# Performance work log

Measured on AMD Instinct MI355X. Metric: run time of the kernel, lower is better.

## Reference

```python
import jax, jax.numpy as jnp
import numpy as np

B, N, DEG = 128, 512, 8          # graphs, nodes per graph, avg degree
E = B * N * DEG                  # 524288 edges
F_IN, H1, H2, C = 128, 64, 128, 10
RATIO = 0.8
K = int(np.ceil(RATIO * N))      # TopKPooling keeps ceil(0.8*N)=410 nodes per graph


def setup_inputs() -> dict:
    key = jax.random.key(0)
    ks = jax.random.split(key, 10)
    n_nodes = B * N
    x = jax.random.normal(ks[0], (n_nodes, F_IN), dtype=jnp.float32)
    # random intra-graph edges, then offset node ids per graph
    src = jax.random.randint(ks[1], (B, N * DEG), 0, N)
    dst = jax.random.randint(ks[2], (B, N * DEG), 0, N)
    off = (jnp.arange(B) * N)[:, None]
    edge_index = jnp.stack([(src + off).reshape(-1), (dst + off).reshape(-1)]).astype(jnp.int64)
    batch = jnp.repeat(jnp.arange(B), N).astype(jnp.int64)
    s1 = 1.0 / np.sqrt(F_IN)
    s2 = 1.0 / np.sqrt(H1)
    s3 = 1.0 / np.sqrt(H2)
    return {
        "x": x,
        "edge_index": edge_index,
        "batch": batch,
        "W1": jax.random.uniform(ks[3], (F_IN, H1), jnp.float32, -s1, s1),
        "b1": jnp.zeros((H1,), jnp.float32),
        "W2": jax.random.uniform(ks[4], (H1, H2), jnp.float32, -s2, s2),
        "b2": jnp.zeros((H2,), jnp.float32),
        "pool_w": jax.random.uniform(ks[5], (H2,), jnp.float32, -s3, s3),
        "fc_W": jax.random.uniform(ks[6], (H2, C), jnp.float32, -s3, s3),
        "fc_b": jax.random.uniform(ks[7], (C,), jnp.float32, -s3, s3),
    }


def gcn_conv(x, W, b, src, dst, num_nodes):
    # PyG GCNConv: add self-loops, symmetric normalization, scatter-add aggregation
    loop = jnp.arange(num_nodes)
    src = jnp.concatenate([src, loop])
    dst = jnp.concatenate([dst, loop])
    deg = jax.ops.segment_sum(jnp.ones_like(src, dtype=x.dtype), dst, num_segments=num_nodes)
    dis = jnp.where(deg > 0, jax.lax.rsqrt(jnp.maximum(deg, 1.0)), 0.0)
    norm = dis[src] * dis[dst]                       # [E+N]
    h = x @ W                                        # transform first (smaller of the two in conv1)
    out = jax.ops.segment_sum(norm[:, None] * h[src], dst, num_segments=num_nodes)
    return out + b


def reference(x, edge_index, batch, W1, b1, W2, b2, pool_w, fc_W, fc_b):
    num_nodes = x.shape[0]
    src, dst = edge_index[0], edge_index[1]
    x = jax.nn.relu(gcn_conv(x, W1, b1, src, dst, num_nodes))
    x = jax.nn.relu(gcn_conv(x, W2, b2, src, dst, num_nodes))
    # TopKPooling: score = (x . w)/||w||, per-graph top-k on raw score, gate by tanh(score)
    score = (x @ pool_w) / jnp.linalg.norm(pool_w)   # [B*N]
    score_b = score.reshape(B, N)
    top_vals, top_idx = jax.lax.top_k(score_b, K)    # [B, K]
    x_b = x.reshape(B, N, H2)
    x_sel = jnp.take_along_axis(x_b, top_idx[:, :, None], axis=1)   # [B, K, H2]
    x_sel = x_sel * jnp.tanh(top_vals)[:, :, None]
    # global max pool over each (pooled) graph; pooled edge_index is unused downstream
    g = jnp.max(x_sel, axis=1)                        # [B, H2]
    logits = g @ fc_W + fc_b                          # [B, C]
    return jax.nn.log_softmax(logits, axis=1)
```

## Files before the change

kernel.cpp:

```cpp
#include <hip/hip_runtime.h>
#include <hip/hip_bf16.h>


#define BB 128
#define NN 512
#define NODES (BB*NN)
#define EE (BB*NN*8)
#define EDGPG (NN*8)
#define F_IN 128
#define H1 64
#define H2 128
#define NC 10
#define KSEL 410
#define ROWCAP 48

typedef unsigned short u16;
typedef unsigned int   u32;

static __device__ __forceinline__ float lo2f(u32 u){ return __uint_as_float(u << 16); }
static __device__ __forceinline__ float hi2f(u32 u){ return __uint_as_float(u & 0xffff0000u); }
static __device__ __forceinline__ u16 f2b(float f){
    __hip_bfloat16 h = __float2bfloat16(f);
    return *reinterpret_cast<u16*>(&h);
}
static __device__ __forceinline__ u32 packbf(float a, float b){
    return (u32)f2b(a) | ((u32)f2b(b) << 16);
}
static __device__ __forceinline__ void acc8s(float* a, uint4 v, float ds){
    a[0] = fmaf(ds, lo2f(v.x), a[0]); a[1] = fmaf(ds, hi2f(v.x), a[1]);
    a[2] = fmaf(ds, lo2f(v.y), a[2]); a[3] = fmaf(ds, hi2f(v.y), a[3]);
    a[4] = fmaf(ds, lo2f(v.z), a[4]); a[5] = fmaf(ds, hi2f(v.z), a[5]);
    a[6] = fmaf(ds, lo2f(v.w), a[6]); a[7] = fmaf(ds, hi2f(v.w), a[7]);
}
static __device__ __forceinline__ void acc8(float* a, uint4 v){
    a[0] += lo2f(v.x); a[1] += hi2f(v.x);
    a[2] += lo2f(v.y); a[3] += hi2f(v.y);
    a[4] += lo2f(v.z); a[5] += hi2f(v.z);
    a[6] += lo2f(v.w); a[7] += hi2f(v.w);
}
static __device__ __forceinline__ int swz2048(int bid){
    return ((bid & 7) << 8) | (bid >> 3);
}

static __device__ __forceinline__ bool ei_is_i64(const int* __restrict__ ei){
    return ((ei[1] | ei[3] | ei[5] | ei[7]) == 0);
}
static __device__ __forceinline__ int ld_src(const int* __restrict__ ei, int e, bool w64){
    return w64 ? ei[2*e] : ei[e];
}
static __device__ __forceinline__ int ld_dst(const int* __restrict__ ei, int e, bool w64){
    return w64 ? ei[2*(EE + e)] : ei[EE + e];
}

#define G1NODES 64
#define XPAD 68
__global__ __launch_bounds__(512) void k_prep_gemm1(const int* __restrict__ ei,
                                                    const float* __restrict__ x,
                                                    const float* __restrict__ W1,
                                                    int* __restrict__ cnt,
                                                    int* __restrict__ adj,
                                                    u32* __restrict__ h1u){
    __shared__ __align__(16) float Ws[64*H1];
    __shared__ __align__(16) float xs[G1NODES*XPAD];
    bool w64 = ei_is_i64(ei);
    int t = threadIdx.x;
    int gb = (int)blockIdx.x;
    int b  = gb >> 3;
    int sub = gb & 7;
    int node0 = b*NN + sub*G1NODES;

    {
        int e = b*EDGPG + sub*512 + t;
        int d = (ld_dst(ei, e, w64) - b*NN) & (NN - 1);
        int s = ld_src(ei, e, w64) & (NODES - 1);
        int node = b*NN + d;
        int p = atomicAdd(&cnt[node], 1);
        if (p < ROWCAP - 1) adj[node*ROWCAP + 1 + p] = s;
    }
    if (t < G1NODES){
        int node = node0 + t;
        adj[node*ROWCAP] = node;
    }

    int tc = t & 15, tr = t >> 4;
    int j0 = tc*4, n0 = tr*2;
    float acc[2][4] = {};
    for (int half = 0; half < 2; ++half){
        const float4* Wv = (const float4*)(W1 + half*4096);
        for (int i = t; i < 1024; i += 512)
            *(float4*)&Ws[i*4] = Wv[i];
        for (int i = t; i < 1024; i += 512){
            int node = i >> 4, c = i & 15;
            float4 v = *(const float4*)(x + (size_t)(node0 + node)*F_IN + half*64 + c*4);
            *(float4*)&xs[node*XPAD + c*4] = v;
        }
        __syncthreads();
        #pragma unroll 2
        for (int k = 0; k < 64; k += 4){
            float4 xv0 = *(const float4*)&xs[(n0+0)*XPAD + k];
            float4 xv1 = *(const float4*)&xs[(n0+1)*XPAD + k];
            float xa0[4] = {xv0.x, xv0.y, xv0.z, xv0.w};
            float xa1[4] = {xv1.x, xv1.y, xv1.z, xv1.w};
            #pragma unroll
            for (int kk = 0; kk < 4; ++kk){
                float4 wv = *(const float4*)&Ws[(k+kk)*H1 + j0];
                acc[0][0] += xa0[kk]*wv.x; acc[0][1] += xa0[kk]*wv.y; acc[0][2] += xa0[kk]*wv.z; acc[0][3] += xa0[kk]*wv.w;
                acc[1][0] += xa1[kk]*wv.x; acc[1][1] += xa1[kk]*wv.y; acc[1][2] += xa1[kk]*wv.z; acc[1][3] += xa1[kk]*wv.w;
            }
        }
        __syncthreads();
    }
    #pragma unroll
    for (int i = 0; i < 2; ++i){
        int node = node0 + n0 + i;
        size_t base = (size_t)node*32 + tc*2;
        h1u[base]     = packbf(acc[i][0], acc[i][1]);
        h1u[base + 1] = packbf(acc[i][2], acc[i][3]);
    }
}

__global__ __launch_bounds__(256) void k_agg1(const uint4* __restrict__ h1v,
                                              const int* __restrict__ cnt,
                                              const int* __restrict__ adj,
                                              const float4* __restrict__ b1v,
                                              uint4* __restrict__ a1v){
    __shared__ float disl[NN];
    int t = threadIdx.x;
    int lb = swz2048((int)blockIdx.x);
    int node0 = lb*32;
    int gbase = node0 & ~(NN - 1);
    for (int i = t; i < NN; i += 256){
        int c = cnt[gbase + i]; if (c > ROWCAP-1) c = ROWCAP-1;
        disl[i] = rsqrtf((float)(c + 1));
    }
    __syncthreads();
    int node = node0 + (t >> 3);
    int fl = t & 7;
    int rs = node*ROWCAP;
    int c = cnt[node]; if (c > ROWCAP-1) c = ROWCAP-1;
    int pe = rs + c + 1;
    float a0[8] = {}, a1r[8] = {}, a2r[8] = {}, a3r[8] = {};
    int p = rs;
    for (; p + 4 <= pe; p += 4){
        int s0 = adj[p], s1 = adj[p+1], s2 = adj[p+2], s3 = adj[p+3];
        float d0 = disl[s0 & (NN-1)], d1 = disl[s1 & (NN-1)];
        float d2 = disl[s2 & (NN-1)], d3 = disl[s3 & (NN-1)];
        uint4 v0 = h1v[s0*8 + fl];
        uint4 v1 = h1v[s1*8 + fl];
        uint4 v2 = h1v[s2*8 + fl];
        uint4 v3 = h1v[s3*8 + fl];
        acc8s(a0, v0, d0); acc8s(a1r, v1, d1); acc8s(a2r, v2, d2); acc8s(a3r, v3, d3);
    }
    for (; p < pe; ++p){
        int s = adj[p];
        acc8s(a0, h1v[s*8 + fl], disl[s & (NN-1)]);
    }
    float r[8];
    #pragma unroll
    for (int j = 0; j < 8; ++j) r[j] = (a0[j] + a1r[j]) + (a2r[j] + a3r[j]);
    float dn = disl[node & (NN-1)];
    float4 bA = b1v[2*fl], bB = b1v[2*fl+1];
    float w0 = dn*r[0] + bA.x; w0 = w0 > 0.f ? w0 : 0.f;
    float w1 = dn*r[1] + bA.y; w1 = w1 > 0.f ? w1 : 0.f;
    float w2 = dn*r[2] + bA.z; w2 = w2 > 0.f ? w2 : 0.f;
    float w3 = dn*r[3] + bA.w; w3 = w3 > 0.f ? w3 : 0.f;
    float w4 = dn*r[4] + bB.x; w4 = w4 > 0.f ? w4 : 0.f;
    float w5 = dn*r[5] + bB.y; w5 = w5 > 0.f ? w5 : 0.f;
    float w6 = dn*r[6] + bB.z; w6 = w6 > 0.f ? w6 : 0.f;
    float w7 = dn*r[7] + bB.w; w7 = w7 > 0.f ? w7 : 0.f;
    a1v[node*8 + fl] = make_uint4(packbf(dn*w0, dn*w1), packbf(dn*w2, dn*w3),
                                  packbf(dn*w4, dn*w5), packbf(dn*w6, dn*w7));
}

#define G2NODES 32
#define APAD 68
__global__ __launch_bounds__(256) void k_gemm2s(const uint4* __restrict__ a1v,
                                                const int* __restrict__ cnt,
                                                const int* __restrict__ adj,
                                                const float* __restrict__ W2,
                                                const float* __restrict__ b2,
                                                const float* __restrict__ pw,
                                                u32* __restrict__ a2u,
                                                float* __restrict__ score){
    __shared__ __align__(16) float Ws[32*H2];
    __shared__ __align__(16) float as[G2NODES*APAD];
    __shared__ float pws[H2];
    int t = threadIdx.x;
    int lb = swz2048((int)blockIdx.x);
    int node0 = lb*G2NODES;
    if (t < H2) pws[t] = pw[t];
    {
        int fl = t & 7, nl = t >> 3;
        int node = node0 + nl;
        int rs = node*ROWCAP;
        int c = cnt[node]; if (c > ROWCAP-1) c = ROWCAP-1;
        int pe = rs + c + 1;
        float a0[8] = {}, a1r[8] = {}, a2r[8] = {}, a3r[8] = {};
        int p = rs;
        for (; p + 4 <= pe; p += 4){
            int s0 = adj[p], s1 = adj[p+1], s2 = adj[p+2], s3 = adj[p+3];
            uint4 v0 = a1v[s0*8 + fl];
            uint4 v1 = a1v[s1*8 + fl];
            uint4 v2 = a1v[s2*8 + fl];
            uint4 v3 = a1v[s3*8 + fl];
            acc8(a0, v0); acc8(a1r, v1); acc8(a2r, v2); acc8(a3r, v3);
        }
        for (; p < pe; ++p){
            uint4 v = a1v[adj[p]*8 + fl];
            acc8(a0, v);
        }
        float dn = rsqrtf((float)(c + 1));
        float* dst = &as[nl*APAD + 8*fl];
        float r0 = dn*((a0[0] + a1r[0]) + (a2r[0] + a3r[0]));
        float r1 = dn*((a0[1] + a1r[1]) + (a2r[1] + a3r[1]));
        float r2 = dn*((a0[2] + a1r[2]) + (a2r[2] + a3r[2]));
        float r3 = dn*((a0[3] + a1r[3]) + (a2r[3] + a3r[3]));
        float r4 = dn*((a0[4] + a1r[4]) + (a2r[4] + a3r[4]));
        float r5 = dn*((a0[5] + a1r[5]) + (a2r[5] + a3r[5]));
        float r6 = dn*((a0[6] + a1r[6]) + (a2r[6] + a3r[6]));
        float r7 = dn*((a0[7] + a1r[7]) + (a2r[7] + a3r[7]));
        *(float4*)&dst[0] = make_float4(r0, r1, r2, r3);
        *(float4*)&dst[4] = make_float4(r4, r5, r6, r7);
    }
    int tc = t & 31, tr = t >> 5;
    int j0 = tc*4, n0 = tr*4;
    float acc[4][4] = {};
    for (int half = 0; half < 2; ++half){
        const float4* Wv = (const float4*)(W2 + half*4096);
        for (int i = t; i < 1024; i += 256)
            *(float4*)&Ws[i*4] = Wv[i];
        __syncthreads();
        int kb = half*32;
        #pragma unroll 2
        for (int k = 0; k < 32; k += 4){
            float4 xv0 = *(const float4*)&as[(n0+0)*APAD + kb + k];
            float4 xv1 = *(const float4*)&as[(n0+1)*APAD + kb + k];
            float4 xv2 = *(const float4*)&as[(n0+2)*APAD + kb + k];
            float4 xv3 = *(const float4*)&as[(n0+3)*APAD + kb + k];
            float xa0[4] = {xv0.x, xv0.y, xv0.z, xv0.w};
            float xa1[4] = {xv1.x, xv1.y, xv1.z, xv1.w};
            float xa2[4] = {xv2.x, xv2.y, xv2.z, xv2.w};
            float xa3[4] = {xv3.x, xv3.y, xv3.z, xv3.w};
            #pragma unroll
            for (int kk = 0; kk < 4; ++kk){
                float4 wv = *(const float4*)&Ws[(k+kk)*H2 + j0];
                acc[0][0] += xa0[kk]*wv.x; acc[0][1] += xa0[kk]*wv.y; acc[0][2] += xa0[kk]*wv.z; acc[0][3] += xa0[kk]*wv.w;
                acc[1][0] += xa1[kk]*wv.x; acc[1][1] += xa1[kk]*wv.y; acc[1][2] += xa1[kk]*wv.z; acc[1][3] += xa1[kk]*wv.w;
                acc[2][0] += xa2[kk]*wv.x; acc[2][1] += xa2[kk]*wv.y; acc[2][2] += xa2[kk]*wv.z; acc[2][3] += xa2[kk]*wv.w;
                acc[3][0] += xa3[kk]*wv.x; acc[3][1] += xa3[kk]*wv.y; acc[3][2] += xa3[kk]*wv.z; acc[3][3] += xa3[kk]*wv.w;
            }
        }
        __syncthreads();
    }
    float p0 = pws[j0], p1 = pws[j0+1], p2 = pws[j0+2], p3 = pws[j0+3];
    float bj0 = b2[j0], bj1 = b2[j0+1], bj2 = b2[j0+2], bj3 = b2[j0+3];
    #pragma unroll
    for (int i = 0; i < 4; ++i){
        float v0 = acc[i][0] + bj0; v0 = v0 > 0.f ? v0 : 0.f;
        float v1 = acc[i][1] + bj1; v1 = v1 > 0.f ? v1 : 0.f;
        float v2 = acc[i][2] + bj2; v2 = v2 > 0.f ? v2 : 0.f;
        float v3 = acc[i][3] + bj3; v3 = v3 > 0.f ? v3 : 0.f;
        size_t base = (size_t)(node0 + n0 + i)*64 + tc*2;
        a2u[base]     = packbf(v0, v1);
        a2u[base + 1] = packbf(v2, v3);
        float sp = v0*p0 + v1*p1 + v2*p2 + v3*p3;
        sp += __shfl_xor(sp, 16, 32);
        sp += __shfl_xor(sp,  8, 32);
        sp += __shfl_xor(sp,  4, 32);
        sp += __shfl_xor(sp,  2, 32);
        sp += __shfl_xor(sp,  1, 32);
        if (tc == 0) score[node0 + n0 + i] = sp;
    }
}

__global__ __launch_bounds__(512) void k_pool(const u32* __restrict__ a2u,
                                              const float* __restrict__ score,
                                              const float* __restrict__ pw,
                                              const float* __restrict__ fcW,
                                              const float* __restrict__ fcb,
                                              float* __restrict__ out){
    __shared__ float so[NN];
    __shared__ float ss[NN];
    __shared__ float th[NN];
    __shared__ float pm[32*H2];
    __shared__ float gl[H2];
    __shared__ float fws[H2*NC];
    __shared__ float lg[NC];
    __shared__ float red[3];
    int b = blockIdx.x, t = threadIdx.x;
    for (int i = t; i < H2*NC; i += 512) fws[i] = fcW[i];
    if (t < H2){ float v = pw[t]; gl[t] = v*v; }
    __syncthreads();
    if (t == 0){
        float s = 0.f;
        for (int i = 0; i < H2; ++i) s += gl[i];
        red[2] = rsqrtf(s);
    }
    __syncthreads();
    float pwinv = red[2];
    float sc = score[b*NN + t];
    so[t] = sc; ss[t] = sc; th[t] = tanhf(sc*pwinv);
    __syncthreads();
    for (int k = 2; k <= NN; k <<= 1){
        for (int j = k >> 1; j > 0; j >>= 1){
            int ixj = t ^ j;
            if (ixj > t){
                float a = ss[t], c = ss[ixj];
                bool desc = ((t & k) == 0);
                bool sw = desc ? (a < c) : (a > c);
                if (sw){ ss[t] = c; ss[ixj] = a; }
            }
            __syncthreads();
        }
    }
    float thresh = ss[KSEL-1];
    float mask_t = (so[t] >= thresh) ? 0.f : -INFINITY;
    __syncthreads();
    so[t] = mask_t;
    __syncthreads();
    int tc = t & 15, q = t >> 4;
    const uint4* ap = (const uint4*)(a2u + (size_t)b*NN*64);
    float m0 = -INFINITY, m1 = -INFINITY, m2 = -INFINITY, m3 = -INFINITY;
    float m4 = -INFINITY, m5 = -INFINITY, m6 = -INFINITY, m7 = -INFINITY;
    int nb = q*16;
    #pragma unroll 4
    for (int n = nb; n < nb + 16; ++n){
        uint4 v = ap[(size_t)n*16 + tc];
        float thn = th[n], son = so[n];
        m0 = fmaxf(m0, lo2f(v.x)*thn + son);
        m1 = fmaxf(m1, hi2f(v.x)*thn + son);
        m2 = fmaxf(m2, lo2f(v.y)*thn + son);
        m3 = fmaxf(m3, hi2f(v.y)*thn + son);
        m4 = fmaxf(m4, lo2f(v.z)*thn + son);
        m5 = fmaxf(m5, hi2f(v.z)*thn + son);
        m6 = fmaxf(m6, lo2f(v.w)*thn + son);
        m7 = fmaxf(m7, hi2f(v.w)*thn + son);
    }
    float* pmr = &pm[q*H2 + 8*tc];
    pmr[0] = m0; pmr[1] = m1; pmr[2] = m2; pmr[3] = m3;
    pmr[4] = m4; pmr[5] = m5; pmr[6] = m6; pmr[7] = m7;
    __syncthreads();
    if (t < H2){
        float g = pm[t];
        #pragma unroll
        for (int qq = 1; qq < 32; ++qq) g = fmaxf(g, pm[qq*H2 + t]);
        gl[t] = g;
    }
    __syncthreads();
    if (t < NC){
        float acc = fcb[t];
        for (int k2 = 0; k2 < H2; ++k2) acc += gl[k2]*fws[k2*NC + t];
        lg[t] = acc;
    }
    __syncthreads();
    if (t == 0){
        float mx = lg[0];
        for (int i = 1; i < NC; ++i) mx = fmaxf(mx, lg[i]);
        float s = 0.f;
        for (int i = 0; i < NC; ++i) s += expf(lg[i] - mx);
        red[0] = mx; red[1] = logf(s);
    }
    __syncthreads();
    if (t < NC) out[b*NC + t] = lg[t] - red[0] - red[1];
}

extern "C" void kernel_launch(void* const* d_in, const int* in_sizes, int n_in,
                              void* d_out, int out_size, void* d_ws, size_t ws_size,
                              hipStream_t stream) {
    const float* x   = (const float*)d_in[0];
    const int*   ei  = (const int*)d_in[1];
    const float* W1  = (const float*)d_in[3];
    const float* b1  = (const float*)d_in[4];
    const float* W2  = (const float*)d_in[5];
    const float* b2  = (const float*)d_in[6];
    const float* pw  = (const float*)d_in[7];
    const float* fcW = (const float*)d_in[8];
    const float* fcb = (const float*)d_in[9];

    char* ws = (char*)d_ws;
    int*   cnt   = (int*)(ws + 4096);
    float* score = (float*)(ws + 524288);
    int*   adj   = (int*)(ws + 4194304);
    u32*   h1u   = (u32*)(ws + 16777216);
    u32*   a1u   = (u32*)(ws + 25165824);
    u32*   a2u   = (u32*)(ws + 33554432);

    hipMemsetAsync(cnt, 0, NODES*sizeof(int), stream);
    k_prep_gemm1<<<NODES/G1NODES, 512, 0, stream>>>(ei, x, W1, cnt, adj, h1u);
    k_agg1<<<NODES/32, 256, 0, stream>>>((const uint4*)h1u, cnt, adj,
                                         (const float4*)b1, (uint4*)a1u);
    k_gemm2s<<<NODES/G2NODES, 256, 0, stream>>>((const uint4*)a1u, cnt, adj,
                                                W2, b2, pw, a2u, score);
    k_pool<<<BB, 512, 0, stream>>>(a2u, score, pw, fcW, fcb, (float*)d_out);
}
```

Baseline: 173.8 us.

## Enlarge per-thread register tiles in both GEMM kernels and vectorize output stores

Each block of the first GEMM kernel (fused with adjacency build) now covers 128 nodes with 256 threads. Each thread computes a 4x8 output tile instead of 2x4 and writes it with one 16-byte store. The second GEMM kernel now covers 64 nodes per block, with two aggregation passes per thread and a 4x8 register tile. Its score reduction shuffles across 16 lanes instead of 32. The aim is more FMAs per shared-memory load, fewer blocks, and wider stores, at the cost of more registers and fewer threads per block, which may reduce occupancy for the gather-heavy aggregation.

After: 176.4 us. About the same (+1.5%).

```diff
diff --git a/kernel.cpp b/kernel.cpp
--- a/kernel.cpp
+++ b/kernel.cpp
@@ -41,6 +41,9 @@
 static __device__ __forceinline__ int swz2048(int bid){
     return ((bid & 7) << 8) | (bid >> 3);
 }
+static __device__ __forceinline__ int swz1024(int bid){
+    return ((bid & 7) << 7) | (bid >> 3);
+}
 
 static __device__ __forceinline__ bool ei_is_i64(const int* __restrict__ ei){
     return ((ei[1] | ei[3] | ei[5] | ei[7]) == 0);
@@ -52,9 +55,9 @@
     return w64 ? ei[2*(EE + e)] : ei[EE + e];
 }
 
-#define G1NODES 64
+#define G1NODES 128
 #define XPAD 68
-__global__ __launch_bounds__(512) void k_prep_gemm1(const int* __restrict__ ei,
+__global__ __launch_bounds__(256) void k_prep_gemm1(const int* __restrict__ ei,
                                                     const float* __restrict__ x,
                                                     const float* __restrict__ W1,
                                                     int* __restrict__ cnt,
@@ -65,12 +68,13 @@
     bool w64 = ei_is_i64(ei);
     int t = threadIdx.x;
     int gb = (int)blockIdx.x;
-    int b  = gb >> 3;
-    int sub = gb & 7;
+    int b  = gb >> 2;
+    int sub = gb & 3;
     int node0 = b*NN + sub*G1NODES;
 
-    {
-        int e = b*EDGPG + sub*512 + t;
+    #pragma unroll
+    for (int i = 0; i < 4; ++i){
+        int e = b*EDGPG + sub*1024 + i*256 + t;
         int d = (ld_dst(ei, e, w64) - b*NN) & (NN - 1);
         int s = ld_src(ei, e, w64) & (NODES - 1);
         int node = b*NN + d;
@@ -82,14 +86,14 @@
         adj[node*ROWCAP] = node;
     }
 
-    int tc = t & 15, tr = t >> 4;
-    int j0 = tc*4, n0 = tr*2;
-    float acc[2][4] = {};
+    int tc = t & 7, tr = t >> 3;
+    int j0 = tc*8;
+    float acc[4][8] = {};
     for (int half = 0; half < 2; ++half){
         const float4* Wv = (const float4*)(W1 + half*4096);
-        for (int i = t; i < 1024; i += 512)
+        for (int i = t; i < 1024; i += 256)
             *(float4*)&Ws[i*4] = Wv[i];
-        for (int i = t; i < 1024; i += 512){
+        for (int i = t; i < 2048; i += 256){
             int node = i >> 4, c = i & 15;
             float4 v = *(const float4*)(x + (size_t)(node0 + node)*F_IN + half*64 + c*4);
             *(float4*)&xs[node*XPAD + c*4] = v;
@@ -97,25 +101,36 @@
         __syncthreads();
         #pragma unroll 2
         for (int k = 0; k < 64; k += 4){
-            float4 xv0 = *(const float4*)&xs[(n0+0)*XPAD + k];
-            float4 xv1 = *(const float4*)&xs[(n0+1)*XPAD + k];
+            float4 xv0 = *(const float4*)&xs[(tr +  0)*XPAD + k];
+            float4 xv1 = *(const float4*)&xs[(tr + 32)*XPAD + k];
+            float4 xv2 = *(const float4*)&xs[(tr + 64)*XPAD + k];
+            float4 xv3 = *(const float4*)&xs[(tr + 96)*XPAD + k];
             float xa0[4] = {xv0.x, xv0.y, xv0.z, xv0.w};
             float xa1[4] = {xv1.x, xv1.y, xv1.z, xv1.w};
+            float xa2[4] = {xv2.x, xv2.y, xv2.z, xv2.w};
+            float xa3[4] = {xv3.x, xv3.y, xv3.z, xv3.w};
             #pragma unroll
             for (int kk = 0; kk < 4; ++kk){
-                float4 wv = *(const float4*)&Ws[(k+kk)*H1 + j0];
-                acc[0][0] += xa0[kk]*wv.x; acc[0][1] += xa0[kk]*wv.y; acc[0][2] += xa0[kk]*wv.z; acc[0][3] += xa0[kk]*wv.w;
-                acc[1][0] += xa1[kk]*wv.x; acc[1][1] += xa1[kk]*wv.y; acc[1][2] += xa1[kk]*wv.z; acc[1][3] += xa1[kk]*wv.w;
+                float4 wa = *(const float4*)&Ws[(k+kk)*H1 + j0];
+                float4 wb = *(const float4*)&Ws[(k+kk)*H1 + j0 + 4];
+                acc[0][0] += xa0[kk]*wa.x; acc[0][1] += xa0[kk]*wa.y; acc[0][2] += xa0[kk]*wa.z; acc[0][3] += xa0[kk]*wa.w;
+                acc[0][4] += xa0[kk]*wb.x; acc[0][5] += xa0[kk]*wb.y; acc[0][6] += xa0[kk]*wb.z; acc[0][7] += xa0[kk]*wb.w;
+                acc[1][0] += xa1[kk]*wa.x; acc[1][1] += xa1[kk]*wa.y; acc[1][2] += xa1[kk]*wa.z; acc[1][3] += xa1[kk]*wa.w;
+                acc[1][4] += xa1[kk]*wb.x; acc[1][5] += xa1[kk]*wb.y; acc[1][6] += xa1[kk]*wb.z; acc[1][7] += xa1[kk]*wb.w;
+                acc[2][0] += xa2[kk]*wa.x; acc[2][1] += xa2[kk]*wa.y; acc[2][2] += xa2[kk]*wa.z; acc[2][3] += xa2[kk]*wa.w;
+                acc[2][4] += xa2[kk]*wb.x; acc[2][5] += xa2[kk]*wb.y; acc[2][6] += xa2[kk]*wb.z; acc[2][7] += xa2[kk]*wb.w;
+                acc[3][0] += xa3[kk]*wa.x; acc[3][1] += xa3[kk]*wa.y; acc[3][2] += xa3[kk]*wa.z; acc[3][3] += xa3[kk]*wa.w;
+                acc[3][4] += xa3[kk]*wb.x; acc[3][5] += xa3[kk]*wb.y; acc[3][6] += xa3[kk]*wb.z; acc[3][7] += xa3[kk]*wb.w;
             }
         }
         __syncthreads();
     }
     #pragma unroll
-    for (int i = 0; i < 2; ++i){
-        int node = node0 + n0 + i;
-        size_t base = (size_t)node*32 + tc*2;
-        h1u[base]     = packbf(acc[i][0], acc[i][1]);
-        h1u[base + 1] = packbf(acc[i][2], acc[i][3]);
+    for (int i = 0; i < 4; ++i){
+        int node = node0 + tr + 32*i;
+        *(uint4*)&h1u[(size_t)node*32 + tc*4] =
+            make_uint4(packbf(acc[i][0], acc[i][1]), packbf(acc[i][2], acc[i][3]),
+                       packbf(acc[i][4], acc[i][5]), packbf(acc[i][6], acc[i][7]));
     }
 }
 
@@ -172,7 +187,7 @@
                                   packbf(dn*w4, dn*w5), packbf(dn*w6, dn*w7));
 }
 
-#define G2NODES 32
+#define G2NODES 64
 #define APAD 68
 __global__ __launch_bounds__(256) void k_gemm2s(const uint4* __restrict__ a1v,
                                                 const int* __restrict__ cnt,
@@ -186,45 +201,48 @@
     __shared__ __align__(16) float as[G2NODES*APAD];
     __shared__ float pws[H2];
     int t = threadIdx.x;
-    int lb = swz2048((int)blockIdx.x);
+    int lb = swz1024((int)blockIdx.x);
     int node0 = lb*G2NODES;
     if (t < H2) pws[t] = pw[t];
     {
-        int fl = t & 7, nl = t >> 3;
-        int node = node0 + nl;
-        int rs = node*ROWCAP;
-        int c = cnt[node]; if (c > ROWCAP-1) c = ROWCAP-1;
-        int pe = rs + c + 1;
-        float a0[8] = {}, a1r[8] = {}, a2r[8] = {}, a3r[8] = {};
-        int p = rs;
-        for (; p + 4 <= pe; p += 4){
-            int s0 = adj[p], s1 = adj[p+1], s2 = adj[p+2], s3 = adj[p+3];
-            uint4 v0 = a1v[s0*8 + fl];
-            uint4 v1 = a1v[s1*8 + fl];
-            uint4 v2 = a1v[s2*8 + fl];
-            uint4 v3 = a1v[s3*8 + fl];
-            acc8(a0, v0); acc8(a1r, v1); acc8(a2r, v2); acc8(a3r, v3);
+        int fl = t & 7, ng = t >> 3;
+        for (int pass = 0; pass < 2; ++pass){
+            int nl = ng + pass*32;
+            int node = node0 + nl;
+            int rs = node*ROWCAP;
+            int c = cnt[node]; if (c > ROWCAP-1) c = ROWCAP-1;
+            int pe = rs + c + 1;
+            float a0[8] = {}, a1r[8] = {}, a2r[8] = {}, a3r[8] = {};
+            int p = rs;
+            for (; p + 4 <= pe; p += 4){
+                int s0 = adj[p], s1 = adj[p+1], s2 = adj[p+2], s3 = adj[p+3];
+                uint4 v0 = a1v[s0*8 + fl];
+                uint4 v1 = a1v[s1*8 + fl];
+                uint4 v2 = a1v[s2*8 + fl];
+                uint4 v3 = a1v[s3*8 + fl];
+                acc8(a0, v0); acc8(a1r, v1); acc8(a2r, v2); acc8(a3r, v3);
+            }
+            for (; p < pe; ++p){
+                uint4 v = a1v[adj[p]*8 + fl];
+                acc8(a0, v);
+            }
+            float dn = rsqrtf((float)(c + 1));
+            float* dst = &as[nl*APAD + 8*fl];
+            float r0 = dn*((a0[0] + a1r[0]) + (a2r[0] + a3r[0]));
+            float r1 = dn*((a0[1] + a1r[1]) + (a2r[1] + a3r[1]));
+            float r2 = dn*((a0[2] + a1r[2]) + (a2r[2] + a3r[2]));
+            float r3 = dn*((a0[3] + a1r[3]) + (a2r[3] + a3r[3]));
+            float r4 = dn*((a0[4] + a1r[4]) + (a2r[4] + a3r[4]));
+            float r5 = dn*((a0[5] + a1r[5]) + (a2r[5] + a3r[5]));
+            float r6 = dn*((a0[6] + a1r[6]) + (a2r[6] + a3r[6]));
+            float r7 = dn*((a0[7] + a1r[7]) + (a2r[7] + a3r[7]));
+            *(float4*)&dst[0] = make_float4(r0, r1, r2, r3);
+            *(float4*)&dst[4] = make_float4(r4, r5, r6, r7);
         }
-        for (; p < pe; ++p){
-            uint4 v = a1v[adj[p]*8 + fl];
-            acc8(a0, v);
-        }
-        float dn = rsqrtf((float)(c + 1));
-        float* dst = &as[nl*APAD + 8*fl];
-        float r0 = dn*((a0[0] + a1r[0]) + (a2r[0] + a3r[0]));
-        float r1 = dn*((a0[1] + a1r[1]) + (a2r[1] + a3r[1]));
-        float r2 = dn*((a0[2] + a1r[2]) + (a2r[2] + a3r[2]));
-        float r3 = dn*((a0[3] + a1r[3]) + (a2r[3] + a3r[3]));
-        float r4 = dn*((a0[4] + a1r[4]) + (a2r[4] + a3r[4]));
-        float r5 = dn*((a0[5] + a1r[5]) + (a2r[5] + a3r[5]));
-        float r6 = dn*((a0[6] + a1r[6]) + (a2r[6] + a3r[6]));
-        float r7 = dn*((a0[7] + a1r[7]) + (a2r[7] + a3r[7]));
-        *(float4*)&dst[0] = make_float4(r0, r1, r2, r3);
-        *(float4*)&dst[4] = make_float4(r4, r5, r6, r7);
-    }
-    int tc = t & 31, tr = t >> 5;
-    int j0 = tc*4, n0 = tr*4;
-    float acc[4][4] = {};
+    }
+    int tc = t & 15, tr = t >> 4;
+    int j0 = tc*8;
+    float acc[4][8] = {};
     for (int half = 0; half < 2; ++half){
         const float4* Wv = (const float4*)(W2 + half*4096);
         for (int i = t; i < 1024; i += 256)
@@ -233,43 +251,54 @@
         int kb = half*32;
         #pragma unroll 2
         for (int k = 0; k < 32; k += 4){
-            float4 xv0 = *(const float4*)&as[(n0+0)*APAD + kb + k];
-            float4 xv1 = *(const float4*)&as[(n0+1)*APAD + kb + k];
-            float4 xv2 = *(const float4*)&as[(n0+2)*APAD + kb + k];
-            float4 xv3 = *(const float4*)&as[(n0+3)*APAD + kb + k];
+            float4 xv0 = *(const float4*)&as[(tr +  0)*APAD + kb + k];
+            float4 xv1 = *(const float4*)&as[(tr + 16)*APAD + kb + k];
+            float4 xv2 = *(const float4*)&as[(tr + 32)*APAD + kb + k];
+            float4 xv3 = *(const float4*)&as[(tr + 48)*APAD + kb + k];
             float xa0[4] = {xv0.x, xv0.y, xv0.z, xv0.w};
             float xa1[4] = {xv1.x, xv1.y, xv1.z, xv1.w};
             float xa2[4] = {xv2.x, xv2.y, xv2.z, xv2.w};
             float xa3[4] = {xv3.x, xv3.y, xv3.z, xv3.w};
             #pragma unroll
             for (int kk = 0; kk < 4; ++kk){
-                float4 wv = *(const float4*)&Ws[(k+kk)*H2 + j0];
-                acc[0][0] += xa0[kk]*wv.x; acc[0][1] += xa0[kk]*wv.y; acc[0][2] += xa0[kk]*wv.z; acc[0][3] += xa0[kk]*wv.w;
-                acc[1][0] += xa1[kk]*wv.x; acc[1][1] += xa1[kk]*wv.y; acc[1][2] += xa1[kk]*wv.z; acc[1][3] += xa1[kk]*wv.w;
-                acc[2][0] += xa2[kk]*wv.x; acc[2][1] += xa2[kk]*wv.y; acc[2][2] += xa2[kk]*wv.z; acc[2][3] += xa2[kk]*wv.w;
-                acc[3][0] += xa3[kk]*wv.x; acc[3][1] += xa3[kk]*wv.y; acc[3][2] += xa3[kk]*wv.z; acc[3][3] += xa3[kk]*wv.w;
+                float4 wa = *(const float4*)&Ws[(k+kk)*H2 + j0];
+                float4 wb = *(const float4*)&Ws[(k+kk)*H2 + j0 + 4];
+                acc[0][0] += xa0[kk]*wa.x; acc[0][1] += xa0[kk]*wa.y; acc[0][2] += xa0[kk]*wa.z; acc[0][3] += xa0[kk]*wa.w;
+                acc[0][4] += xa0[kk]*wb.x; acc[0][5] += xa0[kk]*wb.y; acc[0][6] += xa0[kk]*wb.z; acc[0][7] += xa0[kk]*wb.w;
+                acc[1][0] += xa1[kk]*wa.x; acc[1][1] += xa1[kk]*wa.y; acc[1][2] += xa1[kk]*wa.z; acc[1][3] += xa1[kk]*wa.w;
+                acc[1][4] += xa1[kk]*wb.x; acc[1][5] += xa1[kk]*wb.y; acc[1][6] += xa1[kk]*wb.z; acc[1][7] += xa1[kk]*wb.w;
+                acc[2][0] += xa2[kk]*wa.x; acc[2][1] += xa2[kk]*wa.y; acc[2][2] += xa2[kk]*wa.z; acc[2][3] += xa2[kk]*wa.w;
+                acc[2][4] += xa2[kk]*wb.x; acc[2][5] += xa2[kk]*wb.y; acc[2][6] += xa2[kk]*wb.z; acc[2][7] += xa2[kk]*wb.w;
+                acc[3][0] += xa3[kk]*wa.x; acc[3][1] += xa3[kk]*wa.y; acc[3][2] += xa3[kk]*wa.z; acc[3][3] += xa3[kk]*wa.w;
+                acc[3][4] += xa3[kk]*wb.x; acc[3][5] += xa3[kk]*wb.y; acc[3][6] += xa3[kk]*wb.z; acc[3][7] += xa3[kk]*wb.w;
             }
         }
         __syncthreads();
     }
-    float p0 = pws[j0], p1 = pws[j0+1], p2 = pws[j0+2], p3 = pws[j0+3];
-    float bj0 = b2[j0], bj1 = b2[j0+1], bj2 = b2[j0+2], bj3 = b2[j0+3];
+    float p0 = pws[j0],   p1 = pws[j0+1], p2 = pws[j0+2], p3 = pws[j0+3];
+    float p4 = pws[j0+4], p5 = pws[j0+5], p6 = pws[j0+6], p7 = pws[j0+7];
+    float bj[8];
+    #pragma unroll
+    for (int c2 = 0; c2 < 8; ++c2) bj[c2] = b2[j0 + c2];
     #pragma unroll
     for (int i = 0; i < 4; ++i){
-        float v0 = acc[i][0] + bj0; v0 = v0 > 0.f ? v0 : 0.f;
-        float v1 = acc[i][1] + bj1; v1 = v1 > 0.f ? v1 : 0.f;
-        float v2 = acc[i][2] + bj2; v2 = v2 > 0.f ? v2 : 0.f;
-        float v3 = acc[i][3] + bj3; v3 = v3 > 0.f ? v3 : 0.f;
-        size_t base = (size_t)(node0 + n0 + i)*64 + tc*2;
-        a2u[base]     = packbf(v0, v1);
-        a2u[base + 1] = packbf(v2, v3);
-        float sp = v0*p0 + v1*p1 + v2*p2 + v3*p3;
-        sp += __shfl_xor(sp, 16, 32);
-        sp += __shfl_xor(sp,  8, 32);
-        sp += __shfl_xor(sp,  4, 32);
-        sp += __shfl_xor(sp,  2, 32);
-        sp += __shfl_xor(sp,  1, 32);
-        if (tc == 0) score[node0 + n0 + i] = sp;
+        int node = node0 + tr + 16*i;
+        float v0 = acc[i][0] + bj[0]; v0 = v0 > 0.f ? v0 : 0.f;
+        float v1 = acc[i][1] + bj[1]; v1 = v1 > 0.f ? v1 : 0.f;
+        float v2 = acc[i][2] + bj[2]; v2 = v2 > 0.f ? v2 : 0.f;
+        float v3 = acc[i][3] + bj[3]; v3 = v3 > 0.f ? v3 : 0.f;
+        float v4 = acc[i][4] + bj[4]; v4 = v4 > 0.f ? v4 : 0.f;
+        float v5 = acc[i][5] + bj[5]; v5 = v5 > 0.f ? v5 : 0.f;
+        float v6 = acc[i][6] + bj[6]; v6 = v6 > 0.f ? v6 : 0.f;
+        float v7 = acc[i][7] + bj[7]; v7 = v7 > 0.f ? v7 : 0.f;
+        *(uint4*)&a2u[(size_t)node*64 + tc*4] =
+            make_uint4(packbf(v0, v1), packbf(v2, v3), packbf(v4, v5), packbf(v6, v7));
+        float sp = v0*p0 + v1*p1 + v2*p2 + v3*p3 + v4*p4 + v5*p5 + v6*p6 + v7*p7;
+        sp += __shfl_xor(sp, 8, 16);
+        sp += __shfl_xor(sp, 4, 16);
+        sp += __shfl_xor(sp, 2, 16);
+        sp += __shfl_xor(sp, 1, 16);
+        if (tc == 0) score[node] = sp;
     }
 }
 
@@ -386,7 +415,7 @@
     u32*   a2u   = (u32*)(ws + 33554432);
 
     hipMemsetAsync(cnt, 0, NODES*sizeof(int), stream);
-    k_prep_gemm1<<<NODES/G1NODES, 512, 0, stream>>>(ei, x, W1, cnt, adj, h1u);
+    k_prep_gemm1<<<NODES/G1NODES, 256, 0, stream>>>(ei, x, W1, cnt, adj, h1u);
     k_agg1<<<NODES/32, 256, 0, stream>>>((const uint4*)h1u, cnt, adj,
                                          (const float4*)b1, (uint4*)a1u);
     k_gemm2s<<<NODES/G2NODES, 256, 0, stream>>>((const uint4*)a1u, cnt, adj,
```
